# Performance work log

Hardware: AMD Instinct MI355X
Metric: run time of the kernel (lower is better)

Reference implementation:

```python
import jax, jax.numpy as jnp
import numpy as np

IN_F = 4096
OUT_F = 4096
N = 16384


def setup_inputs() -> dict:
    key = jax.random.key(0)
    kx, kw = jax.random.split(key)
    x = jax.random.normal(kx, (N, IN_F), dtype=jnp.float32)
    # reset_parameters: weight ~ N(0, 1/in_features), bias = 0
    weight = jax.random.normal(kw, (OUT_F, IN_F), dtype=jnp.float32) * (1.0 / np.sqrt(IN_F))
    bias = jnp.zeros((OUT_F,), dtype=jnp.float32)
    return {"x": x, "weight": weight, "bias": bias}


def reference(x, weight, bias):
    # binary_linear_scalar: per-output-row scaling factor alpha = mean(|W|),
    # binarized weight bw = sign(W) * alpha  (XNOR-Net style)
    alpha = jnp.mean(jnp.abs(weight), axis=1, keepdims=True)  # [out, 1]
    bw = jnp.sign(weight) * alpha                             # [out, in]
    # y = x @ bw^T + bias
    return jnp.einsum('ni,oi->no', x, bw) + bias
```

## Files before the change

kernel.cpp:

```cpp
#include <hip/hip_runtime.h>
#include <hip/hip_bf16.h>
#include <stdint.h>

#define IN_F  4096
#define OUT_F 4096
#define NROWS 16384
#define NT    (IN_F / 64)

typedef unsigned short u16;
typedef unsigned int u32;
typedef unsigned long long u64;
typedef __bf16 bf16x8 __attribute__((ext_vector_type(8)));
typedef float  f32x4  __attribute__((ext_vector_type(4)));
typedef u16    u16x8  __attribute__((ext_vector_type(8)));

#define BAR()   asm volatile("s_barrier" ::: "memory")
#define VM4()   asm volatile("s_waitcnt vmcnt(4)" ::: "memory")

__device__ __forceinline__ u16 f2bf(float x) {
    union { float f; uint32_t u; } c; c.f = x;
    uint32_t u = c.u;
    return (u16)((u + 0x7FFFu + ((u >> 16) & 1u)) >> 16);
}

__device__ __forceinline__ void gload_lds16(const void* g, void* l) {
    __builtin_amdgcn_global_load_lds(
        (const __attribute__((address_space(1))) void*)g,
        (__attribute__((address_space(3))) void*)l, 16, 0, 0);
}

__device__ __forceinline__ u16 sgn_bf16(float v) {
    return v > 0.f ? 0x3F80 : (v < 0.f ? 0xBF80 : 0);
}

__global__ void prep_wbits_kernel(const float* __restrict__ W,
                                  float* __restrict__ alpha,
                                  u64* __restrict__ Wbits) {
    const int row = blockIdx.x;
    const int wave = threadIdx.x >> 6, lane = threadIdx.x & 63;
    const float* wr = W + (size_t)row * IN_F;
    float s = 0.f;
#pragma unroll 4
    for (int it = 0; it < 16; ++it) {
        const int kword = it * 4 + wave;
        float v = __builtin_nontemporal_load(wr + kword * 64 + lane);
        s += fabsf(v);
        u64 m = __ballot(v > 0.f);
        if (lane == 0) Wbits[(size_t)kword * OUT_F + row] = m;
    }
    for (int off = 32; off > 0; off >>= 1) s += __shfl_down(s, off);
    __shared__ float red[4];
    if (lane == 0) red[wave] = s;
    __syncthreads();
    if (threadIdx.x == 0)
        alpha[row] = (red[0] + red[1] + red[2] + red[3]) * (1.0f / IN_F);
}

__global__ void convx_kernel(const float* __restrict__ X, u16* __restrict__ O,
                             int swz) {
    const size_t idx = (size_t)blockIdx.x * 256 + threadIdx.x;
    const int row = (int)(idx >> 9);
    const int q = (int)idx & 511;
    const int g = q >> 3, c8 = q & 7;
    const int c8s = swz ? (c8 ^ (row & 7)) : c8;
    const f32x4* src = reinterpret_cast<const f32x4*>(
        X + (size_t)row * IN_F + g * 64 + c8s * 8);
    f32x4 a = __builtin_nontemporal_load(src);
    f32x4 b = __builtin_nontemporal_load(src + 1);
    u16x8 r;
    r[0] = f2bf(a[0]); r[1] = f2bf(a[1]); r[2] = f2bf(a[2]); r[3] = f2bf(a[3]);
    r[4] = f2bf(b[0]); r[5] = f2bf(b[1]); r[6] = f2bf(b[2]); r[7] = f2bf(b[3]);
    reinterpret_cast<u16x8*>(O)[idx] = r;
}

__global__ __launch_bounds__(512, 2) void gemm8_kernel(
    const u16* __restrict__ Xbf, const u64* __restrict__ Wbits,
    const float* __restrict__ alpha, const float* __restrict__ bias,
    float* __restrict__ Y) {
    __shared__ u16 Alds[3][16384];

    const int tid  = threadIdx.x;
    const int lane = tid & 63, wave = tid >> 6;
    const int wm = wave >> 2, wn = wave & 3;
    const int lrow = lane & 15;

    const int wg = blockIdx.x;
    const int i  = wg >> 3;
    const int m0 = (((wg & 7) << 3) | (i >> 4)) << 8;
    const int n0 = (i & 15) << 8;

    const int q0 = ((lane >> 4) << 3) ^ ((lrow & 7) << 3);
    const int q1 = q0 ^ 32;
    const int sh = (lane >> 4) << 3;
    const int brow = n0 + wn * 64 + lrow;

    f32x4 acc[8][4];
#pragma unroll
    for (int a = 0; a < 8; ++a)
#pragma unroll
        for (int b = 0; b < 4; ++b) acc[a][b] = (f32x4){0.f, 0.f, 0.f, 0.f};

    auto stageA = [&](int th, int half, u16* buf) {
        if (th >= NT) return;
#pragma unroll
        for (int t2 = 0; t2 < 2; ++t2) {
            const int c = half * 1024 + t2 * 512 + tid;
            const int row = c >> 3, c8 = c & 7;
            gload_lds16(Xbf + (size_t)(m0 + row) * IN_F + th * 64 + c8 * 8,
                        buf + c * 8);
        }
    };

    u64 wcur[4];
    auto loadbits = [&](int th) {
        if (th >= NT) return;
#pragma unroll
        for (int nf = 0; nf < 4; ++nf)
            wcur[nf] = Wbits[(size_t)th * OUT_F + brow + nf * 16];
    };

    auto expand_pair = [&](u64 w, bf16x8* dst) {
        u64 t64 = w >> sh;
        unsigned nb0 = ~(unsigned)t64;
        unsigned nb1 = ~(unsigned)(t64 >> 32);
        union { unsigned u[4]; bf16x8 v; } r0, r1;
#pragma unroll
        for (int e = 0; e < 4; ++e) {
            unsigned s0 = nb0 >> (2 * e), s1 = nb1 >> (2 * e);
            r0.u[e] = 0x3F803F80u | ((s0 & 1u) << 15) | ((s0 & 2u) << 30);
            r1.u[e] = 0x3F803F80u | ((s1 & 1u) << 15) | ((s1 & 2u) << 30);
        }
        dst[0] = r0.v; dst[1] = r1.v;
    };

    u16* pa0 = &Alds[0][0];
    u16* pa1 = &Alds[1][0];
    u16* pa2 = &Alds[2][0];

    stageA(0, 0, pa0); stageA(0, 1, pa0);
    stageA(1, 0, pa1); stageA(1, 1, pa1);
    loadbits(0);
    VM4(); BAR();

    for (int t = 0; t < NT; ++t) {
        const u16* Ar = pa0 + wm * 8192 + lrow * 64;
        bf16x8 af0[8], af1[8];
#pragma unroll
        for (int mm = 0; mm < 8; ++mm) {
            af0[mm] = *reinterpret_cast<const bf16x8*>(Ar + mm * 1024 + q0);
            af1[mm] = *reinterpret_cast<const bf16x8*>(Ar + mm * 1024 + q1);
        }

        bf16x8 bP[2], bQ[2];
        expand_pair(wcur[0], bP);
        __builtin_amdgcn_s_setprio(1);
#pragma unroll
        for (int mm = 0; mm < 8; ++mm) {
            acc[mm][0] = __builtin_amdgcn_mfma_f32_16x16x32_bf16(af0[mm], bP[0], acc[mm][0], 0, 0, 0);
            acc[mm][0] = __builtin_amdgcn_mfma_f32_16x16x32_bf16(af1[mm], bP[1], acc[mm][0], 0, 0, 0);
        }
        __builtin_amdgcn_s_setprio(0);
        expand_pair(wcur[1], bQ);
        stageA(t + 2, 0, pa2); stageA(t + 2, 1, pa2);
        __builtin_amdgcn_s_setprio(1);
#pragma unroll
        for (int mm = 0; mm < 8; ++mm) {
            acc[mm][1] = __builtin_amdgcn_mfma_f32_16x16x32_bf16(af0[mm], bQ[0], acc[mm][1], 0, 0, 0);
            acc[mm][1] = __builtin_amdgcn_mfma_f32_16x16x32_bf16(af1[mm], bQ[1], acc[mm][1], 0, 0, 0);
        }
        __builtin_amdgcn_s_setprio(0);
        expand_pair(wcur[2], bP);
        __builtin_amdgcn_s_setprio(1);
#pragma unroll
        for (int mm = 0; mm < 8; ++mm) {
            acc[mm][2] = __builtin_amdgcn_mfma_f32_16x16x32_bf16(af0[mm], bP[0], acc[mm][2], 0, 0, 0);
            acc[mm][2] = __builtin_amdgcn_mfma_f32_16x16x32_bf16(af1[mm], bP[1], acc[mm][2], 0, 0, 0);
        }
        __builtin_amdgcn_s_setprio(0);
        expand_pair(wcur[3], bQ);
        loadbits(t + 1);
        __builtin_amdgcn_s_setprio(1);
#pragma unroll
        for (int mm = 0; mm < 8; ++mm) {
            acc[mm][3] = __builtin_amdgcn_mfma_f32_16x16x32_bf16(af0[mm], bQ[0], acc[mm][3], 0, 0, 0);
            acc[mm][3] = __builtin_amdgcn_mfma_f32_16x16x32_bf16(af1[mm], bQ[1], acc[mm][3], 0, 0, 0);
        }
        __builtin_amdgcn_s_setprio(0);

        BAR();

        u16* tp = pa0; pa0 = pa1; pa1 = pa2; pa2 = tp;
    }

#pragma unroll
    for (int nf = 0; nf < 4; ++nf) {
        const int col = n0 + wn * 64 + nf * 16 + lrow;
        const float al = alpha[col], bi = bias[col];
#pragma unroll
        for (int mf = 0; mf < 8; ++mf) {
            const int rbase = m0 + wm * 128 + mf * 16 + ((lane >> 4) << 2);
#pragma unroll
            for (int r = 0; r < 4; ++r)
                __builtin_nontemporal_store(acc[mf][nf][r] * al + bi,
                    &Y[(size_t)(rbase + r) * OUT_F + col]);
        }
    }
}

__global__ void prep_w_kernel(const float* __restrict__ W,
                              float* __restrict__ alpha,
                              u16* __restrict__ S) {
    const int row = blockIdx.x;
    const float* wr = W + (size_t)row * IN_F;
    float s = 0.f;
    for (int c = threadIdx.x; c < 512; c += 256) {
        const f32x4* src = reinterpret_cast<const f32x4*>(wr + c * 8);
        f32x4 v0 = __builtin_nontemporal_load(src);
        f32x4 v1 = __builtin_nontemporal_load(src + 1);
        s += fabsf(v0[0]) + fabsf(v0[1]) + fabsf(v0[2]) + fabsf(v0[3])
           + fabsf(v1[0]) + fabsf(v1[1]) + fabsf(v1[2]) + fabsf(v1[3]);
        u16x8 r;
        r[0] = sgn_bf16(v0[0]); r[1] = sgn_bf16(v0[1]);
        r[2] = sgn_bf16(v0[2]); r[3] = sgn_bf16(v0[3]);
        r[4] = sgn_bf16(v1[0]); r[5] = sgn_bf16(v1[1]);
        r[6] = sgn_bf16(v1[2]); r[7] = sgn_bf16(v1[3]);
        *reinterpret_cast<u16x8*>(S + (size_t)row * IN_F + c * 8) = r;
    }
    for (int off = 32; off > 0; off >>= 1) s += __shfl_down(s, off);
    __shared__ float red[4];
    const int wave = threadIdx.x >> 6, lane = threadIdx.x & 63;
    if (lane == 0) red[wave] = s;
    __syncthreads();
    if (threadIdx.x == 0)
        alpha[row] = (red[0] + red[1] + red[2] + red[3]) * (1.0f / IN_F);
}

__global__ __launch_bounds__(256) void gemm_fallback(
    const float* __restrict__ X, const u16* __restrict__ Wsign,
    const float* __restrict__ alpha, const float* __restrict__ bias,
    float* __restrict__ Y) {
    __shared__ u16 Axl[128 * 64];
    __shared__ u16 Bxl[128 * 64];

    const int tid = threadIdx.x;
    const int n0 = blockIdx.x * 128;
    const int m0 = blockIdx.y * 128;
    const int wave = tid >> 6, lane = tid & 63;
    const int wm = wave >> 1, wn = wave & 1;
    const int lrow = lane & 15;
    const int lk8 = (lane >> 4) * 8;

    f32x4 acc[4][4];
#pragma unroll
    for (int a = 0; a < 4; ++a)
#pragma unroll
        for (int b = 0; b < 4; ++b) acc[a][b] = (f32x4){0.f, 0.f, 0.f, 0.f};

    for (int kt = 0; kt < IN_F; kt += 64) {
#pragma unroll
        for (int j = 0; j < 4; ++j) {
            const int idx = j * 256 + tid;
            const int row = idx >> 3, c8 = idx & 7;
            gload_lds16(Wsign + (size_t)(n0 + row) * IN_F + kt + c8 * 8,
                        &Bxl[idx * 8]);
        }
#pragma unroll
        for (int j = 0; j < 4; ++j) {
            const int idx = j * 256 + tid;
            const int row = idx >> 3, c8 = idx & 7;
            const float* src = X + (size_t)(m0 + row) * IN_F + kt + c8 * 8;
            float4 v0 = *reinterpret_cast<const float4*>(src);
            float4 v1 = *reinterpret_cast<const float4*>(src + 4);
            u16x8 r;
            r[0] = f2bf(v0.x); r[1] = f2bf(v0.y); r[2] = f2bf(v0.z); r[3] = f2bf(v0.w);
            r[4] = f2bf(v1.x); r[5] = f2bf(v1.y); r[6] = f2bf(v1.z); r[7] = f2bf(v1.w);
            *reinterpret_cast<u16x8*>(&Axl[idx * 8]) = r;
        }
        __syncthreads();
#pragma unroll
        for (int kk = 0; kk < 2; ++kk) {
            bf16x8 af[4], bfv[4];
#pragma unroll
            for (int mf = 0; mf < 4; ++mf)
                af[mf] = *reinterpret_cast<const bf16x8*>(
                    &Axl[(wm * 64 + mf * 16 + lrow) * 64 + kk * 32 + lk8]);
#pragma unroll
            for (int nf = 0; nf < 4; ++nf)
                bfv[nf] = *reinterpret_cast<const bf16x8*>(
                    &Bxl[(wn * 64 + nf * 16 + lrow) * 64 + kk * 32 + lk8]);
#pragma unroll
            for (int mf = 0; mf < 4; ++mf)
#pragma unroll
                for (int nf = 0; nf < 4; ++nf)
                    acc[mf][nf] = __builtin_amdgcn_mfma_f32_16x16x32_bf16(
                        af[mf], bfv[nf], acc[mf][nf], 0, 0, 0);
        }
        __syncthreads();
    }
#pragma unroll
    for (int nf = 0; nf < 4; ++nf) {
        const int col = n0 + wn * 64 + nf * 16 + lrow;
        const float al = alpha[col], bi = bias[col];
#pragma unroll
        for (int mf = 0; mf < 4; ++mf) {
            const int rbase = m0 + wm * 64 + mf * 16 + (lane >> 4) * 4;
#pragma unroll
            for (int r = 0; r < 4; ++r)
                __builtin_nontemporal_store(acc[mf][nf][r] * al + bi,
                    &Y[(size_t)(rbase + r) * OUT_F + col]);
        }
    }
}

extern "C" void kernel_launch(void* const* d_in, const int* in_sizes, int n_in,
                              void* d_out, int out_size, void* d_ws, size_t ws_size,
                              hipStream_t stream) {
    const float* X    = (const float*)d_in[0];
    const float* W    = (const float*)d_in[1];
    const float* bias = (const float*)d_in[2];
    float* Y = (float*)d_out;

    char* ws = (char*)d_ws;
    float* alpha = (float*)ws;
    const size_t WBITS_OFF = 16384;
    const size_t XBF_OFF   = WBITS_OFF + (size_t)OUT_F * (IN_F / 8);
    const size_t need_fast = XBF_OFF + (size_t)NROWS * IN_F * 2;

    if (ws_size >= need_fast) {
        u64* Wbits = (u64*)(ws + WBITS_OFF);
        u16* Xbf   = (u16*)(ws + XBF_OFF);
        prep_wbits_kernel<<<OUT_F, 256, 0, stream>>>(W, alpha, Wbits);
        convx_kernel<<<(size_t)NROWS * IN_F / 8 / 256, 256, 0, stream>>>(X, Xbf, 1);
        gemm8_kernel<<<dim3(1024), 512, 0, stream>>>(Xbf, Wbits, alpha, bias, Y);
    } else {
        u16* Wsign = (u16*)(ws + 16384);
        prep_w_kernel<<<OUT_F, 256, 0, stream>>>(W, alpha, Wsign);
        dim3 grid(OUT_F / 128, NROWS / 128);
        gemm_fallback<<<grid, 256, 0, stream>>>(X, Wsign, alpha, bias, Y);
    }
}
```

Measured before the change: 524.7 us.

## Use 4-wave workgroups with 128x128 per-wave tiles and explicit vmcnt waits

The GEMM workgroup drops from 8 waves to 4. Each wave now computes 128 rows by 128 columns, so it holds 64 accumulator fragments instead of 32, and the block tile stays 256x256. Staging loads are redistributed over 256 threads, the weight-bit expansion is software-pipelined one N-fragment ahead, and the loop waits with explicit vmcnt(8), draining to vmcnt(0) on the last two iterations. The larger per-wave tile raises A-fragment reuse but greatly increases register pressure, and launch bounds of 256,1 allow fewer waves in flight to hide latency.

```diff
diff --git a/kernel.cpp b/kernel.cpp
--- a/kernel.cpp
+++ b/kernel.cpp
@@ -15,7 +15,8 @@
 typedef u16    u16x8  __attribute__((ext_vector_type(8)));
 
 #define BAR()   asm volatile("s_barrier" ::: "memory")
-#define VM4()   asm volatile("s_waitcnt vmcnt(4)" ::: "memory")
+#define VM8()   asm volatile("s_waitcnt vmcnt(8)" ::: "memory")
+#define VM0()   asm volatile("s_waitcnt vmcnt(0)" ::: "memory")
 
 __device__ __forceinline__ u16 f2bf(float x) {
     union { float f; uint32_t u; } c; c.f = x;
@@ -73,7 +74,7 @@
     reinterpret_cast<u16x8*>(O)[idx] = r;
 }
 
-__global__ __launch_bounds__(512, 2) void gemm8_kernel(
+__global__ __launch_bounds__(256, 1) void gemm8_kernel(
     const u16* __restrict__ Xbf, const u64* __restrict__ Wbits,
     const float* __restrict__ alpha, const float* __restrict__ bias,
     float* __restrict__ Y) {
@@ -81,7 +82,7 @@
 
     const int tid  = threadIdx.x;
     const int lane = tid & 63, wave = tid >> 6;
-    const int wm = wave >> 2, wn = wave & 3;
+    const int wm = wave >> 1, wn = wave & 1;
     const int lrow = lane & 15;
 
     const int wg = blockIdx.x;
@@ -92,30 +93,30 @@
     const int q0 = ((lane >> 4) << 3) ^ ((lrow & 7) << 3);
     const int q1 = q0 ^ 32;
     const int sh = (lane >> 4) << 3;
-    const int brow = n0 + wn * 64 + lrow;
-
-    f32x4 acc[8][4];
+    const int brow = n0 + wn * 128 + lrow;
+
+    f32x4 acc[8][8];
 #pragma unroll
     for (int a = 0; a < 8; ++a)
 #pragma unroll
-        for (int b = 0; b < 4; ++b) acc[a][b] = (f32x4){0.f, 0.f, 0.f, 0.f};
+        for (int b = 0; b < 8; ++b) acc[a][b] = (f32x4){0.f, 0.f, 0.f, 0.f};
 
     auto stageA = [&](int th, int half, u16* buf) {
         if (th >= NT) return;
 #pragma unroll
-        for (int t2 = 0; t2 < 2; ++t2) {
-            const int c = half * 1024 + t2 * 512 + tid;
+        for (int j = 0; j < 4; ++j) {
+            const int c = half * 1024 + j * 256 + tid;
             const int row = c >> 3, c8 = c & 7;
             gload_lds16(Xbf + (size_t)(m0 + row) * IN_F + th * 64 + c8 * 8,
                         buf + c * 8);
         }
     };
 
-    u64 wcur[4];
+    u64 wcur[8];
     auto loadbits = [&](int th) {
         if (th >= NT) return;
 #pragma unroll
-        for (int nf = 0; nf < 4; ++nf)
+        for (int nf = 0; nf < 8; ++nf)
             wcur[nf] = Wbits[(size_t)th * OUT_F + brow + nf * 16];
     };
 
@@ -137,10 +138,10 @@
     u16* pa1 = &Alds[1][0];
     u16* pa2 = &Alds[2][0];
 
+    loadbits(0);
     stageA(0, 0, pa0); stageA(0, 1, pa0);
     stageA(1, 0, pa1); stageA(1, 1, pa1);
-    loadbits(0);
-    VM4(); BAR();
+    VM8(); BAR();
 
     for (int t = 0; t < NT; ++t) {
         const u16* Ar = pa0 + wm * 8192 + lrow * 64;
@@ -151,50 +152,32 @@
             af1[mm] = *reinterpret_cast<const bf16x8*>(Ar + mm * 1024 + q1);
         }
 
-        bf16x8 bP[2], bQ[2];
-        expand_pair(wcur[0], bP);
-        __builtin_amdgcn_s_setprio(1);
-#pragma unroll
-        for (int mm = 0; mm < 8; ++mm) {
-            acc[mm][0] = __builtin_amdgcn_mfma_f32_16x16x32_bf16(af0[mm], bP[0], acc[mm][0], 0, 0, 0);
-            acc[mm][0] = __builtin_amdgcn_mfma_f32_16x16x32_bf16(af1[mm], bP[1], acc[mm][0], 0, 0, 0);
-        }
-        __builtin_amdgcn_s_setprio(0);
-        expand_pair(wcur[1], bQ);
+        bf16x8 bb[2][2];
+        expand_pair(wcur[0], bb[0]);
+#pragma unroll
+        for (int nf = 0; nf < 8; ++nf) {
+            if (nf < 7) expand_pair(wcur[nf + 1], bb[(nf + 1) & 1]);
+            __builtin_amdgcn_s_setprio(1);
+#pragma unroll
+            for (int mm = 0; mm < 8; ++mm) {
+                acc[mm][nf] = __builtin_amdgcn_mfma_f32_16x16x32_bf16(af0[mm], bb[nf & 1][0], acc[mm][nf], 0, 0, 0);
+                acc[mm][nf] = __builtin_amdgcn_mfma_f32_16x16x32_bf16(af1[mm], bb[nf & 1][1], acc[mm][nf], 0, 0, 0);
+            }
+            __builtin_amdgcn_s_setprio(0);
+        }
+
+        loadbits(t + 1);
         stageA(t + 2, 0, pa2); stageA(t + 2, 1, pa2);
-        __builtin_amdgcn_s_setprio(1);
-#pragma unroll
-        for (int mm = 0; mm < 8; ++mm) {
-            acc[mm][1] = __builtin_amdgcn_mfma_f32_16x16x32_bf16(af0[mm], bQ[0], acc[mm][1], 0, 0, 0);
-            acc[mm][1] = __builtin_amdgcn_mfma_f32_16x16x32_bf16(af1[mm], bQ[1], acc[mm][1], 0, 0, 0);
-        }
-        __builtin_amdgcn_s_setprio(0);
-        expand_pair(wcur[2], bP);
-        __builtin_amdgcn_s_setprio(1);
-#pragma unroll
-        for (int mm = 0; mm < 8; ++mm) {
-            acc[mm][2] = __builtin_amdgcn_mfma_f32_16x16x32_bf16(af0[mm], bP[0], acc[mm][2], 0, 0, 0);
-            acc[mm][2] = __builtin_amdgcn_mfma_f32_16x16x32_bf16(af1[mm], bP[1], acc[mm][2], 0, 0, 0);
-        }
-        __builtin_amdgcn_s_setprio(0);
-        expand_pair(wcur[3], bQ);
-        loadbits(t + 1);
-        __builtin_amdgcn_s_setprio(1);
-#pragma unroll
-        for (int mm = 0; mm < 8; ++mm) {
-            acc[mm][3] = __builtin_amdgcn_mfma_f32_16x16x32_bf16(af0[mm], bQ[0], acc[mm][3], 0, 0, 0);
-            acc[mm][3] = __builtin_amdgcn_mfma_f32_16x16x32_bf16(af1[mm], bQ[1], acc[mm][3], 0, 0, 0);
-        }
-        __builtin_amdgcn_s_setprio(0);
-
+
+        if (t >= NT - 2) { VM0(); } else { VM8(); }
         BAR();
 
         u16* tp = pa0; pa0 = pa1; pa1 = pa2; pa2 = tp;
     }
 
 #pragma unroll
-    for (int nf = 0; nf < 4; ++nf) {
-        const int col = n0 + wn * 64 + nf * 16 + lrow;
+    for (int nf = 0; nf < 8; ++nf) {
+        const int col = n0 + wn * 128 + nf * 16 + lrow;
         const float al = alpha[col], bi = bias[col];
 #pragma unroll
         for (int mf = 0; mf < 8; ++mf) {
@@ -331,7 +314,7 @@
         u16* Xbf   = (u16*)(ws + XBF_OFF);
         prep_wbits_kernel<<<OUT_F, 256, 0, stream>>>(W, alpha, Wbits);
         convx_kernel<<<(size_t)NROWS * IN_F / 8 / 256, 256, 0, stream>>>(X, Xbf, 1);
-        gemm8_kernel<<<dim3(1024), 512, 0, stream>>>(Xbf, Wbits, alpha, bias, Y);
+        gemm8_kernel<<<dim3(1024), 256, 0, stream>>>(Xbf, Wbits, alpha, bias, Y);
     } else {
         u16* Wsign = (u16*)(ws + 16384);
         prep_w_kernel<<<OUT_F, 256, 0, stream>>>(W, alpha, Wsign);
```

Result: slower. 1.836 ms (+249.9%).
